# Kernel tuning notes

Measured on AMD Instinct MI355X. Metric: run time of the kernel, lower is better.

## Reference

```python
import jax, jax.numpy as jnp
import numpy as np

N_NODES = 100000
N_EDGES = 1600000
IN_FEATS = 256
OUT_FEATS = 128


def setup_inputs() -> dict:
    key = jax.random.key(0)
    k1, k2, k3, k4, k5 = jax.random.split(key, 5)
    inputs = jax.random.normal(k1, (N_NODES, IN_FEATS), dtype=jnp.float32)
    # kaiming_uniform-like init for W
    bound = np.sqrt(6.0 / IN_FEATS)
    W = jax.random.uniform(k2, (IN_FEATS, OUT_FEATS), dtype=jnp.float32, minval=-bound, maxval=bound)
    B = jnp.zeros((OUT_FEATS,), dtype=jnp.float32)
    edge_src = jax.random.randint(k3, (N_EDGES,), 0, N_NODES, dtype=jnp.int32)
    edge_dst = jax.random.randint(k4, (N_EDGES,), 0, N_NODES, dtype=jnp.int32)
    # normalized-adjacency-style positive edge weights
    edge_weight = jax.random.uniform(k5, (N_EDGES,), dtype=jnp.float32)
    return {"inputs": inputs, "W": W, "B": B,
            "edge_src": edge_src, "edge_dst": edge_dst, "edge_weight": edge_weight}


def reference(inputs, W, B, edge_src, edge_dst, edge_weight):
    # support = inputs @ W  (dense GEMM)  [N, out_feats]
    support = inputs @ W
    # output = spmm(adj, support): out[dst] += w_e * support[src]
    gathered = support[edge_src] * edge_weight[:, None]        # [E, out_feats]
    output = jax.ops.segment_sum(gathered, edge_dst, num_segments=inputs.shape[0])
    return output + B
```

## Files before the change

kernel.cpp:

```cpp
#include <hip/hip_runtime.h>
#include <cstddef>

#define IN_F 256
#define OUT_F 128
#define SCAN_CHUNK 1024
#define RANGES 8
#define SCHUNKS 512
#define NXCD 8

__global__ __launch_bounds__(256) void gemm_kernel(const float* __restrict__ X,
                                                   const float* __restrict__ W,
                                                   float* __restrict__ S,
                                                   int nrows) {
    __shared__ float Xs[32][68];
    __shared__ float Ws[32][128];
    const int t = threadIdx.x;
    const int bm = blockIdx.x * 64;
    const int tr = (t >> 5) * 8;
    const int tc = (t & 31) * 4;
    float acc[8][4] = {};

    for (int kt = 0; kt < IN_F; kt += 32) {
#pragma unroll
        for (int l = 0; l < 2; ++l) {
            const int idx = t + l * 256;
            const int r = idx >> 3;
            const int k4 = idx & 7;
            int rr = bm + r; if (rr >= nrows) rr = nrows - 1;
            const float4 v = *reinterpret_cast<const float4*>(
                &X[(size_t)rr * IN_F + kt + k4 * 4]);
            Xs[k4 * 4 + 0][r] = v.x;
            Xs[k4 * 4 + 1][r] = v.y;
            Xs[k4 * 4 + 2][r] = v.z;
            Xs[k4 * 4 + 3][r] = v.w;
        }
#pragma unroll
        for (int l = 0; l < 4; ++l) {
            const int q = t + l * 256;
            const int k = q >> 5;
            const int c = (q & 31) * 4;
            *reinterpret_cast<float4*>(&Ws[k][c]) =
                *reinterpret_cast<const float4*>(&W[(size_t)(kt + k) * OUT_F + c]);
        }
        __syncthreads();
#pragma unroll 4
        for (int kk = 0; kk < 32; ++kk) {
            const float4 x0 = *reinterpret_cast<const float4*>(&Xs[kk][tr]);
            const float4 x1 = *reinterpret_cast<const float4*>(&Xs[kk][tr + 4]);
            const float4 wv = *reinterpret_cast<const float4*>(&Ws[kk][tc]);
            const float xr8[8] = {x0.x, x0.y, x0.z, x0.w, x1.x, x1.y, x1.z, x1.w};
#pragma unroll
            for (int j = 0; j < 8; ++j) {
                acc[j][0] += xr8[j] * wv.x;
                acc[j][1] += xr8[j] * wv.y;
                acc[j][2] += xr8[j] * wv.z;
                acc[j][3] += xr8[j] * wv.w;
            }
        }
        __syncthreads();
    }
#pragma unroll
    for (int j = 0; j < 8; ++j) {
        const int row = bm + tr + j;
        if (row < nrows) {
            *reinterpret_cast<float4*>(&S[(size_t)row * OUT_F + tc]) =
                make_float4(acc[j][0], acc[j][1], acc[j][2], acc[j][3]);
        }
    }
}

__global__ void hist_kernel(const int* __restrict__ dst, int* __restrict__ counts, int E) {
    int i = blockIdx.x * blockDim.x + threadIdx.x;
    const int stride = gridDim.x * blockDim.x;
    for (; i < E; i += stride) atomicAdd(&counts[dst[i]], 1);
}

__global__ __launch_bounds__(256) void scan1_kernel(const int* __restrict__ counts,
                                                    int* __restrict__ off,
                                                    int* __restrict__ bsums, int n) {
    __shared__ int sd[256];
    const int t = threadIdx.x;
    const int base = blockIdx.x * SCAN_CHUNK + t * 4;
    int c[4]; int s = 0;
#pragma unroll
    for (int j = 0; j < 4; ++j) {
        c[j] = (base + j < n) ? counts[base + j] : 0;
        s += c[j];
    }
    sd[t] = s;
    __syncthreads();
    for (int d = 1; d < 256; d <<= 1) {
        int v = (t >= d) ? sd[t - d] : 0;
        __syncthreads();
        sd[t] += v;
        __syncthreads();
    }
    int run = sd[t] - s;
#pragma unroll
    for (int j = 0; j < 4; ++j) {
        if (base + j < n) off[base + j] = run;
        run += c[j];
    }
    if (t == 255) bsums[blockIdx.x] = sd[255];
}

__global__ __launch_bounds__(256) void scan2_kernel(int* __restrict__ bsums, int nb) {
    __shared__ int sd[256];
    const int t = threadIdx.x;
    const int v = (t < nb) ? bsums[t] : 0;
    sd[t] = v;
    __syncthreads();
    for (int d = 1; d < 256; d <<= 1) {
        int u = (t >= d) ? sd[t - d] : 0;
        __syncthreads();
        sd[t] += u;
        __syncthreads();
    }
    if (t < nb) bsums[t] = sd[t] - v;
}

__global__ __launch_bounds__(256) void scan3_kernel(int* __restrict__ off,
                                                    int* __restrict__ cursor,
                                                    const int* __restrict__ bsums,
                                                    int n, int total) {
    const int t = threadIdx.x;
    const int base = blockIdx.x * SCAN_CHUNK + t * 4;
    const int add = bsums[blockIdx.x];
#pragma unroll
    for (int j = 0; j < 4; ++j) {
        const int idx = base + j;
        if (idx < n) {
            const int v = off[idx] + add;
            off[idx] = v;
            cursor[idx] = v;
        }
    }
    if (blockIdx.x == 0 && t == 0) off[n] = total;
}

__global__ __launch_bounds__(256) void scatter_kernel(const int* __restrict__ src,
                                                      const int* __restrict__ dst,
                                                      const float* __restrict__ w,
                                                      int* __restrict__ cursor,
                                                      int2* __restrict__ pairs,
                                                      int E, int nodes_per_range) {
    const int range = blockIdx.x % NXCD;
    const int chunk = blockIdx.x / NXCD;
    const int r_lo = range * nodes_per_range;
    const int r_hi = r_lo + nodes_per_range;
    const int per_chunk = (E + SCHUNKS - 1) / SCHUNKS;
    const int start = chunk * per_chunk;
    const int end = min(E, start + per_chunk);
    for (int i = start + threadIdx.x; i < end; i += 256) {
        const int d = dst[i];
        if (d >= r_lo && d < r_hi) {
            const int pos = atomicAdd(&cursor[d], 1);
            int2 p;
            p.x = src[i];
            p.y = __float_as_int(w[i]);
            pairs[pos] = p;
        }
    }
}

__global__ __launch_bounds__(256) void gather_kernel(const float* __restrict__ S,
                                                     const int* __restrict__ off,
                                                     const int2* __restrict__ pairs,
                                                     const float* __restrict__ B,
                                                     float* __restrict__ out, int n) {
    const int node = blockIdx.x * 4 + (threadIdx.x >> 6);
    const int lane = threadIdx.x & 63;
    if (node >= n) return;
    const int s = off[node];
    const int e = off[node + 1];
    const size_t fo = (size_t)lane * 2;
    float a0x = 0.f, a0y = 0.f, a1x = 0.f, a1y = 0.f;
    float a2x = 0.f, a2y = 0.f, a3x = 0.f, a3y = 0.f;
    int i = s;
    for (; i + 8 <= e; i += 8) {
        const int2 p0 = pairs[i];
        const int2 p1 = pairs[i + 1];
        const int2 p2 = pairs[i + 2];
        const int2 p3 = pairs[i + 3];
        const int2 p4 = pairs[i + 4];
        const int2 p5 = pairs[i + 5];
        const int2 p6 = pairs[i + 6];
        const int2 p7 = pairs[i + 7];
        const float2 v0 = *reinterpret_cast<const float2*>(&S[(size_t)p0.x * OUT_F + fo]);
        const float2 v1 = *reinterpret_cast<const float2*>(&S[(size_t)p1.x * OUT_F + fo]);
        const float2 v2 = *reinterpret_cast<const float2*>(&S[(size_t)p2.x * OUT_F + fo]);
        const float2 v3 = *reinterpret_cast<const float2*>(&S[(size_t)p3.x * OUT_F + fo]);
        const float2 v4 = *reinterpret_cast<const float2*>(&S[(size_t)p4.x * OUT_F + fo]);
        const float2 v5 = *reinterpret_cast<const float2*>(&S[(size_t)p5.x * OUT_F + fo]);
        const float2 v6 = *reinterpret_cast<const float2*>(&S[(size_t)p6.x * OUT_F + fo]);
        const float2 v7 = *reinterpret_cast<const float2*>(&S[(size_t)p7.x * OUT_F + fo]);
        a0x += __int_as_float(p0.y) * v0.x; a0y += __int_as_float(p0.y) * v0.y;
        a1x += __int_as_float(p1.y) * v1.x; a1y += __int_as_float(p1.y) * v1.y;
        a2x += __int_as_float(p2.y) * v2.x; a2y += __int_as_float(p2.y) * v2.y;
        a3x += __int_as_float(p3.y) * v3.x; a3y += __int_as_float(p3.y) * v3.y;
        a0x += __int_as_float(p4.y) * v4.x; a0y += __int_as_float(p4.y) * v4.y;
        a1x += __int_as_float(p5.y) * v5.x; a1y += __int_as_float(p5.y) * v5.y;
        a2x += __int_as_float(p6.y) * v6.x; a2y += __int_as_float(p6.y) * v6.y;
        a3x += __int_as_float(p7.y) * v7.x; a3y += __int_as_float(p7.y) * v7.y;
    }
    if (i + 4 <= e) {
        const int2 p0 = pairs[i];
        const int2 p1 = pairs[i + 1];
        const int2 p2 = pairs[i + 2];
        const int2 p3 = pairs[i + 3];
        const float2 v0 = *reinterpret_cast<const float2*>(&S[(size_t)p0.x * OUT_F + fo]);
        const float2 v1 = *reinterpret_cast<const float2*>(&S[(size_t)p1.x * OUT_F + fo]);
        const float2 v2 = *reinterpret_cast<const float2*>(&S[(size_t)p2.x * OUT_F + fo]);
        const float2 v3 = *reinterpret_cast<const float2*>(&S[(size_t)p3.x * OUT_F + fo]);
        a0x += __int_as_float(p0.y) * v0.x; a0y += __int_as_float(p0.y) * v0.y;
        a1x += __int_as_float(p1.y) * v1.x; a1y += __int_as_float(p1.y) * v1.y;
        a2x += __int_as_float(p2.y) * v2.x; a2y += __int_as_float(p2.y) * v2.y;
        a3x += __int_as_float(p3.y) * v3.x; a3y += __int_as_float(p3.y) * v3.y;
        i += 4;
    }
    for (; i < e; ++i) {
        const int2 p = pairs[i];
        const float2 v = *reinterpret_cast<const float2*>(&S[(size_t)p.x * OUT_F + fo]);
        const float wv = __int_as_float(p.y);
        a0x += wv * v.x; a0y += wv * v.y;
    }
    const float2 b2 = *reinterpret_cast<const float2*>(&B[fo]);
    float2 o;
    o.x = (a0x + a1x) + (a2x + a3x) + b2.x;
    o.y = (a0y + a1y) + (a2y + a3y) + b2.y;
    *reinterpret_cast<float2*>(&out[(size_t)node * OUT_F + fo]) = o;
}

__global__ void init_out_kernel(float* __restrict__ out, const float* __restrict__ B, size_t n) {
    size_t i = (size_t)blockIdx.x * blockDim.x + threadIdx.x;
    const size_t stride = (size_t)gridDim.x * blockDim.x;
    for (; i < n; i += stride) out[i] = B[i & (OUT_F - 1)];
}

__global__ void atomic_scatter_kernel(const float* __restrict__ S, const int* __restrict__ src,
                                      const int* __restrict__ dst, const float* __restrict__ w,
                                      float* __restrict__ out, int E) {
    size_t i = (size_t)blockIdx.x * blockDim.x + threadIdx.x;
    const size_t stride = (size_t)gridDim.x * blockDim.x;
    const size_t total = (size_t)E * OUT_F;
    for (; i < total; i += stride) {
        const int e = (int)(i >> 7);
        const int f = (int)(i & 127);
        atomicAdd(&out[(size_t)dst[e] * OUT_F + f], w[e] * S[(size_t)src[e] * OUT_F + f]);
    }
}

extern "C" void kernel_launch(void* const* d_in, const int* in_sizes, int n_in,
                              void* d_out, int out_size, void* d_ws, size_t ws_size,
                              hipStream_t stream) {
    const float* X    = (const float*)d_in[0];
    const float* W    = (const float*)d_in[1];
    const float* B    = (const float*)d_in[2];
    const int*   esrc = (const int*)d_in[3];
    const int*   edst = (const int*)d_in[4];
    const float* ew   = (const float*)d_in[5];
    float* out = (float*)d_out;

    const int N = in_sizes[0] / IN_F;
    const int E = in_sizes[3];

    char* ws = (char*)d_ws;
    size_t cur = 0;
    auto carve = [&](size_t bytes) -> void* {
        void* p = ws + cur;
        cur = (cur + bytes + 255) & ~(size_t)255;
        return p;
    };
    float* support = (float*)carve((size_t)N * OUT_F * sizeof(float));
    int*   counts  = (int*)carve((size_t)N * sizeof(int));
    int*   offs    = (int*)carve((size_t)(N + 1) * sizeof(int));
    int*   cursor  = (int*)carve((size_t)N * sizeof(int));
    int*   bsums   = (int*)carve(1024 * sizeof(int));
    int2*  pairs   = (int2*)carve((size_t)E * sizeof(int2));
    const bool csr_ok = (cur <= ws_size);

    const int gemm_grid = (N + 63) / 64;
    gemm_kernel<<<gemm_grid, 256, 0, stream>>>(X, W, support, N);

    if (csr_ok) {
        hipMemsetAsync(counts, 0, (size_t)N * sizeof(int), stream);
        hist_kernel<<<2048, 256, 0, stream>>>(edst, counts, E);
        const int nb = (N + SCAN_CHUNK - 1) / SCAN_CHUNK;
        scan1_kernel<<<nb, 256, 0, stream>>>(counts, offs, bsums, N);
        scan2_kernel<<<1, 256, 0, stream>>>(bsums, nb);
        scan3_kernel<<<nb, 256, 0, stream>>>(offs, cursor, bsums, N, E);
        const int npr = (N + RANGES - 1) / RANGES;
        scatter_kernel<<<SCHUNKS * NXCD, 256, 0, stream>>>(esrc, edst, ew, cursor, pairs, E, npr);
        gather_kernel<<<(N + 3) / 4, 256, 0, stream>>>(support, offs, pairs, B, out, N);
    } else {
        init_out_kernel<<<2048, 256, 0, stream>>>(out, B, (size_t)N * OUT_F);
        atomic_scatter_kernel<<<4096, 256, 0, stream>>>(support, esrc, edst, ew, out, E);
    }
}
```

Baseline: 500.8 us.

## Bucket edges by destination range before CSR placement; enlarge GEMM tile

Replaces the histogram pass and the 8-way range-filtered scatter with a bucket kernel. The bucket kernel stages edge chunks in LDS, counts destinations, and writes edges into per-range buckets. A place kernel then reads each bucket only once to scatter pairs into CSR order, where previously every range pass rescanned all edges. The GEMM tile also grows from 64x128 to 128x128 with 8x8 per-thread accumulators to raise arithmetic intensity. This costs extra workspace for the bucket buffers, more registers in the GEMM, and a bucket capacity that could overflow on skewed inputs.

```diff
diff --git a/kernel.cpp b/kernel.cpp
--- a/kernel.cpp
+++ b/kernel.cpp
@@ -5,24 +5,26 @@
 #define OUT_F 128
 #define SCAN_CHUNK 1024
 #define RANGES 8
+#define NXCD 8
+#define ACHUNK 2048
+#define PB_CHUNKS 256
 #define SCHUNKS 512
-#define NXCD 8
 
 __global__ __launch_bounds__(256) void gemm_kernel(const float* __restrict__ X,
                                                    const float* __restrict__ W,
                                                    float* __restrict__ S,
                                                    int nrows) {
-    __shared__ float Xs[32][68];
+    __shared__ float Xs[32][132];
     __shared__ float Ws[32][128];
     const int t = threadIdx.x;
-    const int bm = blockIdx.x * 64;
-    const int tr = (t >> 5) * 8;
-    const int tc = (t & 31) * 4;
-    float acc[8][4] = {};
+    const int bm = blockIdx.x * 128;
+    const int tr = (t >> 4) * 8;
+    const int tc = (t & 15) * 8;
+    float acc[8][8] = {};
 
     for (int kt = 0; kt < IN_F; kt += 32) {
 #pragma unroll
-        for (int l = 0; l < 2; ++l) {
+        for (int l = 0; l < 4; ++l) {
             const int idx = t + l * 256;
             const int r = idx >> 3;
             const int k4 = idx & 7;
@@ -43,18 +45,18 @@
                 *reinterpret_cast<const float4*>(&W[(size_t)(kt + k) * OUT_F + c]);
         }
         __syncthreads();
-#pragma unroll 4
+#pragma unroll 2
         for (int kk = 0; kk < 32; ++kk) {
-            const float4 x0 = *reinterpret_cast<const float4*>(&Xs[kk][tr]);
-            const float4 x1 = *reinterpret_cast<const float4*>(&Xs[kk][tr + 4]);
-            const float4 wv = *reinterpret_cast<const float4*>(&Ws[kk][tc]);
-            const float xr8[8] = {x0.x, x0.y, x0.z, x0.w, x1.x, x1.y, x1.z, x1.w};
+            const float4 xa = *reinterpret_cast<const float4*>(&Xs[kk][tr]);
+            const float4 xb = *reinterpret_cast<const float4*>(&Xs[kk][tr + 4]);
+            const float4 wa = *reinterpret_cast<const float4*>(&Ws[kk][tc]);
+            const float4 wb = *reinterpret_cast<const float4*>(&Ws[kk][tc + 4]);
+            const float xr8[8] = {xa.x, xa.y, xa.z, xa.w, xb.x, xb.y, xb.z, xb.w};
+            const float wc8[8] = {wa.x, wa.y, wa.z, wa.w, wb.x, wb.y, wb.z, wb.w};
 #pragma unroll
             for (int j = 0; j < 8; ++j) {
-                acc[j][0] += xr8[j] * wv.x;
-                acc[j][1] += xr8[j] * wv.y;
-                acc[j][2] += xr8[j] * wv.z;
-                acc[j][3] += xr8[j] * wv.w;
+#pragma unroll
+                for (int i = 0; i < 8; ++i) acc[j][i] += xr8[j] * wc8[i];
             }
         }
         __syncthreads();
@@ -65,14 +67,71 @@
         if (row < nrows) {
             *reinterpret_cast<float4*>(&S[(size_t)row * OUT_F + tc]) =
                 make_float4(acc[j][0], acc[j][1], acc[j][2], acc[j][3]);
-        }
-    }
-}
-
-__global__ void hist_kernel(const int* __restrict__ dst, int* __restrict__ counts, int E) {
-    int i = blockIdx.x * blockDim.x + threadIdx.x;
-    const int stride = gridDim.x * blockDim.x;
-    for (; i < E; i += stride) atomicAdd(&counts[dst[i]], 1);
+            *reinterpret_cast<float4*>(&S[(size_t)row * OUT_F + tc + 4]) =
+                make_float4(acc[j][4], acc[j][5], acc[j][6], acc[j][7]);
+        }
+    }
+}
+
+__global__ __launch_bounds__(256) void bucket_kernel(const int* __restrict__ src,
+                                                     const int* __restrict__ dst,
+                                                     const float* __restrict__ w,
+                                                     int* __restrict__ counts,
+                                                     int* __restrict__ btails,
+                                                     int2* __restrict__ bsrcw,
+                                                     int* __restrict__ bdst,
+                                                     int E, int npr, int bcap) {
+    __shared__ int sdst[ACHUNK];
+    __shared__ int ssrc[ACHUNK];
+    __shared__ float swt[ACHUNK];
+    __shared__ int bcnt[RANGES], bbase[RANGES], bcur[RANGES];
+    const int t = threadIdx.x;
+    const int start = blockIdx.x * ACHUNK;
+    const int cnt = min(ACHUNK, E - start);
+    if (t < RANGES) { bcnt[t] = 0; bcur[t] = 0; }
+    for (int j = t; j < cnt; j += 256) {
+        sdst[j] = dst[start + j];
+        ssrc[j] = src[start + j];
+        swt[j] = w[start + j];
+    }
+    __syncthreads();
+    for (int j = t; j < cnt; j += 256) {
+        const int d = sdst[j];
+        atomicAdd(&bcnt[(unsigned)d / (unsigned)npr], 1);
+        atomicAdd(&counts[d], 1);
+    }
+    __syncthreads();
+    if (t < RANGES) bbase[t] = atomicAdd(&btails[t], bcnt[t]);
+    __syncthreads();
+    for (int j = t; j < cnt; j += 256) {
+        const int d = sdst[j];
+        const int r = (unsigned)d / (unsigned)npr;
+        const int loc = atomicAdd(&bcur[r], 1);
+        const size_t pos = (size_t)r * bcap + bbase[r] + loc;
+        bsrcw[pos] = make_int2(ssrc[j], __float_as_int(swt[j]));
+        bdst[pos] = d;
+    }
+}
+
+__global__ __launch_bounds__(256) void place_kernel(const int2* __restrict__ bsrcw,
+                                                    const int* __restrict__ bdst,
+                                                    const int* __restrict__ btails,
+                                                    int* __restrict__ cursor,
+                                                    int2* __restrict__ pairs,
+                                                    int bcap) {
+    const int r = blockIdx.x & (RANGES - 1);
+    const int chunk = blockIdx.x >> 3;
+    const int sz = btails[r];
+    const int per = (sz + PB_CHUNKS - 1) / PB_CHUNKS;
+    const int s = chunk * per;
+    const int e = min(sz, s + per);
+    const size_t base = (size_t)r * bcap;
+    for (int i = s + threadIdx.x; i < e; i += 256) {
+        const int2 sw = bsrcw[base + i];
+        const int d = bdst[base + i];
+        const int pos = atomicAdd(&cursor[d], 1);
+        pairs[pos] = sw;
+    }
 }
 
 __global__ __launch_bounds__(256) void scan1_kernel(const int* __restrict__ counts,
@@ -161,6 +220,12 @@
             pairs[pos] = p;
         }
     }
+}
+
+__global__ void hist_kernel(const int* __restrict__ dst, int* __restrict__ counts, int E) {
+    int i = blockIdx.x * blockDim.x + threadIdx.x;
+    const int stride = gridDim.x * blockDim.x;
+    for (; i < E; i += stride) atomicAdd(&counts[dst[i]], 1);
 }
 
 __global__ __launch_bounds__(256) void gather_kernel(const float* __restrict__ S,
@@ -276,13 +341,33 @@
     int*   offs    = (int*)carve((size_t)(N + 1) * sizeof(int));
     int*   cursor  = (int*)carve((size_t)N * sizeof(int));
     int*   bsums   = (int*)carve(1024 * sizeof(int));
+    int*   btails  = (int*)carve(RANGES * sizeof(int));
     int2*  pairs   = (int2*)carve((size_t)E * sizeof(int2));
-    const bool csr_ok = (cur <= ws_size);
-
-    const int gemm_grid = (N + 63) / 64;
+    const size_t base_need = cur;
+    const int bcap = E / RANGES + 16384;
+    int2*  bsrcw   = (int2*)carve((size_t)RANGES * bcap * sizeof(int2));
+    int*   bdst    = (int*)carve((size_t)RANGES * bcap * sizeof(int));
+    const bool bucket_ok = (cur <= ws_size);
+    const bool csr_ok = (base_need <= ws_size);
+
+    const int gemm_grid = (N + 127) / 128;
     gemm_kernel<<<gemm_grid, 256, 0, stream>>>(X, W, support, N);
 
-    if (csr_ok) {
+    if (bucket_ok) {
+        hipMemsetAsync(counts, 0, (size_t)N * sizeof(int), stream);
+        hipMemsetAsync(btails, 0, RANGES * sizeof(int), stream);
+        const int npr = (N + RANGES - 1) / RANGES;
+        const int na = (E + ACHUNK - 1) / ACHUNK;
+        bucket_kernel<<<na, 256, 0, stream>>>(esrc, edst, ew, counts, btails,
+                                              bsrcw, bdst, E, npr, bcap);
+        const int nb = (N + SCAN_CHUNK - 1) / SCAN_CHUNK;
+        scan1_kernel<<<nb, 256, 0, stream>>>(counts, offs, bsums, N);
+        scan2_kernel<<<1, 256, 0, stream>>>(bsums, nb);
+        scan3_kernel<<<nb, 256, 0, stream>>>(offs, cursor, bsums, N, E);
+        place_kernel<<<RANGES * PB_CHUNKS, 256, 0, stream>>>(bsrcw, bdst, btails,
+                                                             cursor, pairs, bcap);
+        gather_kernel<<<(N + 3) / 4, 256, 0, stream>>>(support, offs, pairs, B, out, N);
+    } else if (csr_ok) {
         hipMemsetAsync(counts, 0, (size_t)N * sizeof(int), stream);
         hist_kernel<<<2048, 256, 0, stream>>>(edst, counts, E);
         const int nb = (N + SCAN_CHUNK - 1) / SCAN_CHUNK;
```

Measured after the change: 510.1 us. Within noise of the previous version (+1.9%).
